# Optimization experiments

Hardware: AMD Instinct MI355X
Metric: run time of the kernel (lower is better)

The kernel has to match this reference:

```python
import jax, jax.numpy as jnp
import numpy as np
import math

N = 4096
E = 131072
D_IN = 148      # d_node_feat
D_HID = 128     # d_node_reshape (DIHGNN.d_node_feat)
D_OUT = 148     # d_output


def setup_inputs() -> dict:
    key = jax.random.key(0)
    ks = jax.random.split(key, 10)
    node_feat = jax.random.normal(ks[0], (1, N, D_IN), dtype=jnp.float32)
    edge_index = jax.random.randint(ks[1], (2, E), 0, N, dtype=jnp.int64)
    # learned parameters
    W1 = jax.random.normal(ks[2], (D_HID, D_IN), dtype=jnp.float32) * 0.02
    b1 = jnp.zeros((D_HID,), dtype=jnp.float32)
    a_param = jnp.array([0.9], dtype=jnp.float32)   # DIHGNN.a
    Wd = jax.random.normal(ks[3], (D_OUT, D_HID), dtype=jnp.float32) * 0.02
    bd = jnp.zeros((D_OUT,), dtype=jnp.float32)
    W2 = jax.random.normal(ks[4], (2, D_OUT), dtype=jnp.float32) * 0.02
    b2 = jnp.zeros((2,), dtype=jnp.float32)
    return {"node_feat": node_feat, "edge_index": edge_index, "num_node": N,
            "W1": W1, "b1": b1, "a_param": a_param, "Wd": Wd, "bd": bd,
            "W2": W2, "b2": b2}


def reference(node_feat, edge_index, num_node, W1, b1, a_param, Wd, bd, W2, b2):
    n = num_node
    x = node_feat[0]                                   # [N, D_IN]
    x = x @ W1.T + b1                                  # linear_1 -> [N, D_HID]

    # dense adjacency via scatter-set (duplicates collapse to 1, as in torch)
    adj = jnp.zeros((n, n), dtype=jnp.float32).at[edge_index[0], edge_index[1]].set(1.0)

    # asymmetric degree normalization: D_col^{-1/2} A D_row^{-1/2}
    L = adj.sum(axis=0)                                # column sums
    R = adj.sum(axis=1)                                # row sums
    L_is = jnp.where(L > 0, jax.lax.rsqrt(jnp.maximum(L, 1e-30)), 0.0)
    R_is = jnp.where(R > 0, jax.lax.rsqrt(jnp.maximum(R, 1e-30)), 0.0)
    adj_norm = L_is[:, None] * adj * R_is[None, :]

    # custom tanh: 0.5 + 0.5 * tanh(2 * a)
    alpha = 0.5 + 0.5 * jnp.tanh(2.0 * a_param[0])     # scalar

    # graph diffusion: (I - alpha * A_norm)^{-1} x, as a linear solve
    eye = jnp.eye(n, dtype=jnp.float32)
    x = jnp.linalg.solve(eye - alpha * adj_norm, x)    # [N, D_HID]

    x = x @ Wd.T + bd                                  # DIHGNN.linear -> [N, D_OUT]

    # similarity loss (scaled by DIHGNN.d_node_feat = D_HID)
    sim = (x @ x.T) / math.sqrt(D_HID)                 # [N, N]
    sim = sim * (1.0 - eye)                            # zero diagonal
    sim = jax.nn.relu(sim)
    loss = sim.sum() / (n * (n - 1))

    x = x * (1.0 - alpha)
    x = jax.nn.relu(x)
    pooled = jnp.max(x, axis=0, keepdims=True)         # global_max_pool, single graph -> [1, D_OUT]
    out = pooled @ W2.T + b2                           # [1, 2]
    return (out, loss)
```

## Files before the change

### kernel.cpp

```cpp
#include <hip/hip_runtime.h>
#include <hip/hip_bf16.h>
#include <math.h>

#define N_NODES 4096
#define N_EDGES 131072
#define BCAP 80
#define DIN 148
#define DHID 128
#define DOUT 148
#define KP 160
#define NITER 6

typedef __attribute__((ext_vector_type(8))) _Float16 half8;
typedef __attribute__((ext_vector_type(4))) float f32x4;

__device__ inline float h2f(unsigned e) {
    union { unsigned short u; _Float16 h; } cv;
    cv.u = (unsigned short)(e & 0xffffu);
    return (float)cv.h;
}
__device__ inline float2 h2f2(unsigned p) {
    union { unsigned u; _Float16 h[2]; } cv; cv.u = p;
    return make_float2((float)cv.h[0], (float)cv.h[1]);
}
__device__ inline unsigned f2h2(float x, float y) {
    union { unsigned u; _Float16 h[2]; } cv;
    cv.h[0] = (_Float16)x; cv.h[1] = (_Float16)y;
    return cv.u;
}

__global__ __launch_bounds__(256) void prep_kernel(const int* __restrict__ ei,
                                                   const float* __restrict__ W1,
                                                   const float* __restrict__ Wd,
                                                   float* __restrict__ W1T,
                                                   float* __restrict__ WdT,
                                                   unsigned* __restrict__ bitmap,
                                                   unsigned* __restrict__ bucket,
                                                   int* __restrict__ rowdeg,
                                                   int* __restrict__ coldeg) {
    int gtid = blockIdx.x * 256 + threadIdx.x;
    if (gtid < DIN * DHID) {
        int kk = gtid >> 7, d = gtid & 127;
        W1T[gtid] = W1[d * DIN + kk];
    } else if (gtid < DIN * DHID + DHID * DOUT) {
        int i2 = gtid - DIN * DHID;
        int h = i2 / DOUT, o = i2 - h * DOUT;
        WdT[i2] = Wd[o * DHID + h];
    }
    int i = ei[gtid] & (N_NODES - 1);
    int j = ei[gtid + N_EDGES] & (N_NODES - 1);
    unsigned pos = (unsigned)i * (unsigned)N_NODES + (unsigned)j;
    unsigned w = pos >> 5, m = 1u << (pos & 31u);
    unsigned old = atomicOr(&bitmap[w], m);
    if (!(old & m)) {
        int p = atomicAdd(&rowdeg[i], 1);
        if (p < BCAP) bucket[i * BCAP + p] = (unsigned)j;
        atomicAdd(&coldeg[j], 1);
    }
}

__global__ __launch_bounds__(256) void finalize_kernel(unsigned* __restrict__ bucket,
                                                       const int* __restrict__ rowdeg,
                                                       const int* __restrict__ coldeg,
                                                       float* __restrict__ acoef,
                                                       const float* __restrict__ a_param,
                                                       const float* __restrict__ nf,
                                                       const float* __restrict__ W1T,
                                                       const float* __restrict__ b1,
                                                       float* __restrict__ Bm,
                                                       unsigned* __restrict__ Bh) {
    int tid = threadIdx.x, bid = blockIdx.x;
    int r0 = bid * 16;
    for (int idx = tid; idx < 16 * BCAP; idx += 256) {
        int r = r0 + idx / BCAP, q = idx % BCAP;
        int dg = min(rowdeg[r], BCAP);
        if (q < dg) {
            unsigned col = bucket[r * BCAP + q];
            int rd = rowdeg[col];
            float rsj = (rd > 0) ? rsqrtf((float)rd) : 0.0f;
            union { _Float16 h; unsigned short u; } cv;
            cv.h = (_Float16)rsj;
            bucket[r * BCAP + q] = (col << 16) | (unsigned)cv.u;
        }
    }
    if (tid < 16) {
        int r = r0 + tid;
        float alpha = 0.5f + 0.5f * tanhf(2.0f * a_param[0]);
        int cd = coldeg[r];
        acoef[r] = (cd > 0) ? alpha * rsqrtf((float)cd) : 0.0f;
    }
    __shared__ float sA[16 * 152];
    __shared__ float sB[16 * 128];
    for (int idx = tid; idx < 16 * DIN; idx += 256) {
        int nd = idx / DIN, c = idx - nd * DIN;
        sA[nd * 152 + c] = nf[(r0 + nd) * DIN + c];
    }
    __syncthreads();
    int half = tid >> 7, d = tid & 127;
    float a[8];
#pragma unroll
    for (int n = 0; n < 8; ++n) a[n] = 0.f;
    const float* sb8 = sA + half * 8 * 152;
    for (int kk = 0; kk < DIN; ++kk) {
        float wv = W1T[kk * DHID + d];
#pragma unroll
        for (int n = 0; n < 8; ++n) a[n] += sb8[n * 152 + kk] * wv;
    }
    float bb = b1[d];
#pragma unroll
    for (int n = 0; n < 8; ++n) {
        int nd = half * 8 + n;
        float v = a[n] + bb;
        Bm[(r0 + nd) * DHID + d] = v;
        sB[nd * 128 + d] = v;
    }
    __syncthreads();
    for (int idx = tid; idx < 16 * 64; idx += 256) {
        int nd = idx >> 6, dp = idx & 63;
        Bh[(r0 + nd) * 64 + dp] = f2h2(sB[nd * 128 + 2 * dp], sB[nd * 128 + 2 * dp + 1]);
    }
}

template<bool INH, bool OUTH, bool LAST>
__global__ __launch_bounds__(256) void spmv_kernel(const void* __restrict__ xin_,
                                                   void* __restrict__ xout_,
                                                   const float* __restrict__ Bm,
                                                   const float* __restrict__ prev2,
                                                   const unsigned* __restrict__ cc,
                                                   const int* __restrict__ rowdeg,
                                                   const float* __restrict__ acoef,
                                                   double* __restrict__ accd) {
    int tid = threadIdx.x;
    int wid = __builtin_amdgcn_readfirstlane(tid >> 6);
    int lane = tid & 63;
    int r = blockIdx.x * 4 + wid;
    int dg8 = (min(rowdeg[r], BCAP) + 7) & ~7;
    int nch = dg8 >> 3;
    const uint4* __restrict__ q = (const uint4*)(cc + r * BCAP);
    const unsigned* __restrict__ xh = (const unsigned*)xin_;
    const float2* __restrict__ x2 = (const float2*)xin_;
    auto ldx = [&](unsigned e) -> float2 {
        int col = (int)(e >> 16);
        if constexpr (INH) return h2f2(xh[col * 64 + lane]);
        else return x2[col * 64 + lane];
    };
    float ax = 0.f, ay = 0.f;
    uint4 qa0 = q[0], qb0 = q[1];
    float2 v0 = ldx(qa0.x), v1 = ldx(qa0.y), v2 = ldx(qa0.z), v3 = ldx(qa0.w);
    float2 v4 = ldx(qb0.x), v5 = ldx(qb0.y), v6 = ldx(qb0.z), v7 = ldx(qb0.w);
    uint4 qa1 = q[2], qb1 = q[3];
    for (int c = 0; c < nch; ++c) {
        float2 w0 = ldx(qa1.x), w1 = ldx(qa1.y), w2 = ldx(qa1.z), w3 = ldx(qa1.w);
        float2 w4 = ldx(qb1.x), w5 = ldx(qb1.y), w6 = ldx(qb1.z), w7 = ldx(qb1.w);
        uint4 na = q[2 * c + 4], nb = q[2 * c + 5];
        float c0 = h2f(qa0.x), c1 = h2f(qa0.y), c2f = h2f(qa0.z), c3 = h2f(qa0.w);
        float c4 = h2f(qb0.x), c5 = h2f(qb0.y), c6 = h2f(qb0.z), c7 = h2f(qb0.w);
        ax += c0 * v0.x + c1 * v1.x + c2f * v2.x + c3 * v3.x
            + c4 * v4.x + c5 * v5.x + c6 * v6.x + c7 * v7.x;
        ay += c0 * v0.y + c1 * v1.y + c2f * v2.y + c3 * v3.y
            + c4 * v4.y + c5 * v5.y + c6 * v6.y + c7 * v7.y;
        qa0 = qa1; qb0 = qb1; qa1 = na; qb1 = nb;
        v0 = w0; v1 = w1; v2 = w2; v3 = w3;
        v4 = w4; v5 = w5; v6 = w6; v7 = w7;
    }
    float ac = acoef[r];
    int idx = r * 64 + lane;
    float2 b = ((const float2*)Bm)[idx];
    float vx = b.x + ac * ax, vy = b.y + ac * ay;
    if constexpr (OUTH) {
        ((unsigned*)xout_)[idx] = f2h2(vx, vy);
    } else {
        ((float2*)xout_)[idx] = make_float2(vx, vy);
    }
    if constexpr (LAST) {
        float2 xp = ((const float2*)xin_)[idx];
        float2 p2 = ((const float2*)prev2)[idx];
        float dpx = xp.x - p2.x, dpy = xp.y - p2.y;
        float dnx = vx - xp.x, dny = vy - xp.y;
        double s0 = (double)dpx * dpx + (double)dpy * dpy;
        double s1 = (double)dnx * dpx + (double)dny * dpy;
        __shared__ double sh0[256], sh1[256];
        sh0[tid] = s0; sh1[tid] = s1;
        __syncthreads();
        for (int off = 128; off > 0; off >>= 1) {
            if (tid < off) { sh0[tid] += sh0[tid + off]; sh1[tid] += sh1[tid + off]; }
            __syncthreads();
        }
        if (tid == 0) { atomicAdd(&accd[1], sh0[0]); atomicAdd(&accd[2], sh1[0]); }
    }
}

__global__ __launch_bounds__(256) void post_kernel(const float* __restrict__ last,
                                                   const float* __restrict__ prev,
                                                   const double* __restrict__ accd,
                                                   const float* __restrict__ WdT,
                                                   const float* __restrict__ bd,
                                                   _Float16* __restrict__ yH,
                                                   unsigned* __restrict__ mcolu) {
    int tid = threadIdx.x, bid = blockIdx.x;
    int r0 = bid * 16;
    double d0 = accd[1], d1 = accd[2];
    float lam = (d0 > 0.0) ? (float)(d1 / d0) : 0.0f;
    float den = 1.0f - lam;
    if (fabsf(den) < 1e-4f) den = (den < 0.0f) ? -1e-4f : 1e-4f;
    float sf = fminf(fmaxf(lam / den, -1e4f), 1e4f);
    __shared__ float sx[16 * DHID];
    for (int idx = tid; idx < 16 * DHID; idx += 256) {
        int node = r0 + (idx >> 7), ccol = idx & 127;
        float l = last[node * DHID + ccol];
        sx[idx] = l + sf * (l - prev[node * DHID + ccol]);
    }
    __syncthreads();
    for (int idx = tid; idx < 16 * (KP - DOUT); idx += 256) {
        int node = r0 + idx / (KP - DOUT);
        int ccol = DOUT + idx % (KP - DOUT);
        yH[node * KP + ccol] = (_Float16)0.0f;
    }
    if (tid < DOUT) {
        float acc[16];
#pragma unroll
        for (int nd = 0; nd < 16; ++nd) acc[nd] = 0.f;
        for (int h = 0; h < DHID; ++h) {
            float wv = WdT[h * DOUT + tid];
#pragma unroll
            for (int nd = 0; nd < 16; ++nd) acc[nd] += sx[nd * DHID + h] * wv;
        }
        float bb = bd[tid];
        float lm = 0.0f;
#pragma unroll
        for (int nd = 0; nd < 16; ++nd) {
            float v = acc[nd] + bb;
            yH[(r0 + nd) * KP + tid] = (_Float16)v;
            lm = fmaxf(lm, v);
        }
        atomicMax(&mcolu[tid], __float_as_uint(lm));
    }
}

__global__ __launch_bounds__(256) void simloss_kernel(const _Float16* __restrict__ yH,
                                                      double* __restrict__ accd,
                                                      unsigned* __restrict__ cnt,
                                                      const unsigned* __restrict__ mcolu,
                                                      const float* __restrict__ W2,
                                                      const float* __restrict__ b2,
                                                      const float* __restrict__ a_param,
                                                      float* __restrict__ out) {
    int tid = threadIdx.x;
    int tb = blockIdx.x;
    int ti = 0, rem = tb;
    while (rem >= 32 - ti) { rem -= 32 - ti; ++ti; }
    int tj = ti + rem;
    int wid = tid >> 6, lane = tid & 63;
    int wr = wid >> 1, wc = wid & 1;
    int fr = lane & 15, kq = lane >> 4;
    const half8* __restrict__ ap =
        (const half8*)(yH + (size_t)(ti * 128 + wr * 64 + fr) * KP);
    const half8* __restrict__ bp =
        (const half8*)(yH + (size_t)(tj * 128 + wc * 64 + fr) * KP);
    f32x4 C[4][4];
#pragma unroll
    for (int m = 0; m < 4; ++m)
#pragma unroll
        for (int n = 0; n < 4; ++n) C[m][n] = (f32x4)0.0f;
#pragma unroll
    for (int kk = 0; kk < KP / 32; ++kk) {
        half8 a[4], bf[4];
#pragma unroll
        for (int m = 0; m < 4; ++m) a[m] = ap[m * 320 + kk * 4 + kq];
#pragma unroll
        for (int n = 0; n < 4; ++n) bf[n] = bp[n * 320 + kk * 4 + kq];
#pragma unroll
        for (int m = 0; m < 4; ++m)
#pragma unroll
            for (int n = 0; n < 4; ++n)
                C[m][n] = __builtin_amdgcn_mfma_f32_16x16x32_f16(a[m], bf[n], C[m][n], 0, 0, 0);
    }
    const float inv = 0.0883883476483184405f;
    float wgt = (ti == tj) ? 1.0f : 2.0f;
    float lsum = 0.0f;
    int rq = kq * 4;
#pragma unroll
    for (int m = 0; m < 4; ++m)
#pragma unroll
        for (int n = 0; n < 4; ++n)
#pragma unroll
            for (int reg = 0; reg < 4; ++reg) {
                int gi = ti * 128 + wr * 64 + m * 16 + rq + reg;
                int gj = tj * 128 + wc * 64 + n * 16 + fr;
                float v = C[m][n][reg] * inv;
                if (gi != gj && v > 0.0f) lsum += wgt * v;
            }
    for (int o2 = 32; o2 > 0; o2 >>= 1) lsum += __shfl_down(lsum, o2);
    __shared__ float ws[4];
    __shared__ bool lastblk;
    if ((tid & 63) == 0) ws[tid >> 6] = lsum;
    __syncthreads();
    if (tid == 0) {
        atomicAdd(&accd[0], (double)(ws[0] + ws[1] + ws[2] + ws[3]));
        __threadfence();
        unsigned r = __hip_atomic_fetch_add(&cnt[1], 1u, __ATOMIC_ACQ_REL,
                                            __HIP_MEMORY_SCOPE_AGENT);
        lastblk = (r == 527u);
    }
    __syncthreads();
    if (lastblk && tid < 64) {
        float alpha = 0.5f + 0.5f * tanhf(2.0f * a_param[0]);
        float oma = 1.0f - alpha;
        float s0 = 0.0f, s1 = 0.0f;
        for (int o = tid; o < DOUT; o += 64) {
            float p = __uint_as_float(mcolu[o]);
            s0 += p * W2[o];
            s1 += p * W2[DOUT + o];
        }
        for (int off = 32; off > 0; off >>= 1) {
            s0 += __shfl_down(s0, off);
            s1 += __shfl_down(s1, off);
        }
        if (tid == 0) {
            double loss = __hip_atomic_load(&accd[0], __ATOMIC_RELAXED,
                                            __HIP_MEMORY_SCOPE_AGENT);
            out[0] = b2[0] + oma * s0;
            out[1] = b2[1] + oma * s1;
            out[2] = (float)(loss / (4096.0 * 4095.0));
        }
    }
}

extern "C" void kernel_launch(void* const* d_in, const int* in_sizes, int n_in,
                              void* d_out, int out_size, void* d_ws, size_t ws_size,
                              hipStream_t stream) {
    (void)in_sizes; (void)n_in; (void)out_size; (void)ws_size;
    const float* node_feat  = (const float*)d_in[0];
    const int*   edge_index = (const int*)d_in[1];
    const float* W1         = (const float*)d_in[3];
    const float* b1         = (const float*)d_in[4];
    const float* a_param    = (const float*)d_in[5];
    const float* Wd         = (const float*)d_in[6];
    const float* bd         = (const float*)d_in[7];
    const float* W2         = (const float*)d_in[8];
    const float* b2         = (const float*)d_in[9];
    float*       out        = (float*)d_out;

    char* w = (char*)d_ws;
    size_t off = 0;
    auto alloc = [&](size_t bytes) -> char* {
        char* p = w + off;
        off = (off + bytes + 255) & ~(size_t)255;
        return p;
    };
    double*   accd    = (double*)   alloc(8 * sizeof(double));
    unsigned* cnt     = (unsigned*) alloc(16 * sizeof(unsigned));
    int*      rowdeg  = (int*)      alloc(N_NODES * 4);
    int*      coldeg  = (int*)      alloc(N_NODES * 4);
    unsigned* mcolu   = (unsigned*) alloc(256 * 4);
    unsigned* bitmap  = (unsigned*) alloc((size_t)N_NODES * N_NODES / 8);
    unsigned* bucket  = (unsigned*) alloc((size_t)N_NODES * BCAP * 4 + 1024);
    size_t zero_end = off;
    float*    acoef   = (float*)    alloc(N_NODES * 4);
    float*    W1T     = (float*)    alloc(DIN * DHID * 4);
    float*    WdT     = (float*)    alloc(DHID * DOUT * 4);
    float*    Bm      = (float*)    alloc(N_NODES * DHID * 4);
    unsigned* Bh      = (unsigned*) alloc((size_t)N_NODES * 64 * 4);
    unsigned* H0      = (unsigned*) alloc((size_t)N_NODES * 64 * 4);
    unsigned* H1      = (unsigned*) alloc((size_t)N_NODES * 64 * 4);
    float*    Y0      = (float*)    alloc(N_NODES * DHID * 4);
    float*    Y1      = (float*)    alloc(N_NODES * DHID * 4);
    float*    Y2      = (float*)    alloc(N_NODES * DHID * 4);
    _Float16* yH      = (_Float16*) alloc((size_t)N_NODES * KP * 2);

    hipMemsetAsync(w, 0, zero_end, stream);

    prep_kernel<<<N_EDGES / 256, 256, 0, stream>>>(edge_index, W1, Wd, W1T, WdT,
                                                   bitmap, bucket, rowdeg, coldeg);
    finalize_kernel<<<N_NODES / 16, 256, 0, stream>>>(bucket, rowdeg, coldeg, acoef,
                                                      a_param, node_feat, W1T, b1, Bm, Bh);

    const int GB = N_NODES / 4;
    spmv_kernel<true,  true,  false><<<GB, 256, 0, stream>>>(Bh, H0, Bm, nullptr, bucket, rowdeg, acoef, accd);
    spmv_kernel<true,  true,  false><<<GB, 256, 0, stream>>>(H0, H1, Bm, nullptr, bucket, rowdeg, acoef, accd);
    spmv_kernel<true,  true,  false><<<GB, 256, 0, stream>>>(H1, H0, Bm, nullptr, bucket, rowdeg, acoef, accd);
    spmv_kernel<true,  false, false><<<GB, 256, 0, stream>>>(H0, Y0, Bm, nullptr, bucket, rowdeg, acoef, accd);
    spmv_kernel<false, false, false><<<GB, 256, 0, stream>>>(Y0, Y1, Bm, nullptr, bucket, rowdeg, acoef, accd);
    spmv_kernel<false, false, true ><<<GB, 256, 0, stream>>>(Y1, Y2, Bm, Y0, bucket, rowdeg, acoef, accd);

    post_kernel<<<N_NODES / 16, 256, 0, stream>>>(Y2, Y1, accd, WdT, bd, yH, mcolu);
    simloss_kernel<<<528, 256, 0, stream>>>(yH, accd, cnt, mcolu, W2, b2, a_param, out);
}
```

Measured before the change: 157.3 us.

## Fuse finalize into prep kernel and compute normalization coefficients inside SpMV

```diff
diff --git a/kernel.cpp b/kernel.cpp
--- a/kernel.cpp
+++ b/kernel.cpp
@@ -9,16 +9,10 @@
 #define DHID 128
 #define DOUT 148
 #define KP 160
-#define NITER 6
 
 typedef __attribute__((ext_vector_type(8))) _Float16 half8;
 typedef __attribute__((ext_vector_type(4))) float f32x4;
 
-__device__ inline float h2f(unsigned e) {
-    union { unsigned short u; _Float16 h; } cv;
-    cv.u = (unsigned short)(e & 0xffffu);
-    return (float)cv.h;
-}
 __device__ inline float2 h2f2(unsigned p) {
     union { unsigned u; _Float16 h[2]; } cv; cv.u = p;
     return make_float2((float)cv.h[0], (float)cv.h[1]);
@@ -28,152 +22,142 @@
     cv.h[0] = (_Float16)x; cv.h[1] = (_Float16)y;
     return cv.u;
 }
+__device__ inline float2 cvtx(unsigned g) { return h2f2(g); }
+__device__ inline float2 cvtx(float2 g)   { return g; }
 
 __global__ __launch_bounds__(256) void prep_kernel(const int* __restrict__ ei,
                                                    const float* __restrict__ W1,
                                                    const float* __restrict__ Wd,
-                                                   float* __restrict__ W1T,
+                                                   const float* __restrict__ b1,
+                                                   const float* __restrict__ nf,
                                                    float* __restrict__ WdT,
                                                    unsigned* __restrict__ bitmap,
                                                    unsigned* __restrict__ bucket,
                                                    int* __restrict__ rowdeg,
-                                                   int* __restrict__ coldeg) {
-    int gtid = blockIdx.x * 256 + threadIdx.x;
-    if (gtid < DIN * DHID) {
-        int kk = gtid >> 7, d = gtid & 127;
-        W1T[gtid] = W1[d * DIN + kk];
-    } else if (gtid < DIN * DHID + DHID * DOUT) {
-        int i2 = gtid - DIN * DHID;
-        int h = i2 / DOUT, o = i2 - h * DOUT;
-        WdT[i2] = Wd[o * DHID + h];
-    }
-    int i = ei[gtid] & (N_NODES - 1);
-    int j = ei[gtid + N_EDGES] & (N_NODES - 1);
-    unsigned pos = (unsigned)i * (unsigned)N_NODES + (unsigned)j;
-    unsigned w = pos >> 5, m = 1u << (pos & 31u);
-    unsigned old = atomicOr(&bitmap[w], m);
-    if (!(old & m)) {
-        int p = atomicAdd(&rowdeg[i], 1);
-        if (p < BCAP) bucket[i * BCAP + p] = (unsigned)j;
-        atomicAdd(&coldeg[j], 1);
-    }
-}
-
-__global__ __launch_bounds__(256) void finalize_kernel(unsigned* __restrict__ bucket,
-                                                       const int* __restrict__ rowdeg,
-                                                       const int* __restrict__ coldeg,
-                                                       float* __restrict__ acoef,
-                                                       const float* __restrict__ a_param,
-                                                       const float* __restrict__ nf,
-                                                       const float* __restrict__ W1T,
-                                                       const float* __restrict__ b1,
-                                                       float* __restrict__ Bm,
-                                                       unsigned* __restrict__ Bh) {
+                                                   int* __restrict__ coldeg,
+                                                   float* __restrict__ Bm,
+                                                   unsigned* __restrict__ Bh) {
     int tid = threadIdx.x, bid = blockIdx.x;
-    int r0 = bid * 16;
-    for (int idx = tid; idx < 16 * BCAP; idx += 256) {
-        int r = r0 + idx / BCAP, q = idx % BCAP;
-        int dg = min(rowdeg[r], BCAP);
-        if (q < dg) {
-            unsigned col = bucket[r * BCAP + q];
-            int rd = rowdeg[col];
-            float rsj = (rd > 0) ? rsqrtf((float)rd) : 0.0f;
-            union { _Float16 h; unsigned short u; } cv;
-            cv.h = (_Float16)rsj;
-            bucket[r * BCAP + q] = (col << 16) | (unsigned)cv.u;
-        }
-    }
-    if (tid < 16) {
-        int r = r0 + tid;
-        float alpha = 0.5f + 0.5f * tanhf(2.0f * a_param[0]);
-        int cd = coldeg[r];
-        acoef[r] = (cd > 0) ? alpha * rsqrtf((float)cd) : 0.0f;
+    int gtid = bid * 256 + tid;
+    if (gtid < DHID * DOUT) {
+        int h = gtid / DOUT, o = gtid - h * DOUT;
+        WdT[gtid] = Wd[o * DHID + h];
+    }
+    {
+        int i = ei[gtid] & (N_NODES - 1);
+        int j = ei[gtid + N_EDGES] & (N_NODES - 1);
+        unsigned pos = (unsigned)i * (unsigned)N_NODES + (unsigned)j;
+        unsigned w = pos >> 5, m = 1u << (pos & 31u);
+        unsigned old = atomicOr(&bitmap[w], m);
+        if (!(old & m)) {
+            int p = atomicAdd(&rowdeg[i], 1);
+            if (p < BCAP) bucket[i * BCAP + p] = (unsigned)j;
+            atomicAdd(&coldeg[j], 1);
+        }
     }
     __shared__ float sA[16 * 152];
     __shared__ float sB[16 * 128];
-    for (int idx = tid; idx < 16 * DIN; idx += 256) {
-        int nd = idx / DIN, c = idx - nd * DIN;
-        sA[nd * 152 + c] = nf[(r0 + nd) * DIN + c];
-    }
-    __syncthreads();
-    int half = tid >> 7, d = tid & 127;
-    float a[8];
-#pragma unroll
-    for (int n = 0; n < 8; ++n) a[n] = 0.f;
-    const float* sb8 = sA + half * 8 * 152;
-    for (int kk = 0; kk < DIN; ++kk) {
-        float wv = W1T[kk * DHID + d];
-#pragma unroll
-        for (int n = 0; n < 8; ++n) a[n] += sb8[n * 152 + kk] * wv;
-    }
-    float bb = b1[d];
-#pragma unroll
-    for (int n = 0; n < 8; ++n) {
-        int nd = half * 8 + n;
-        float v = a[n] + bb;
-        Bm[(r0 + nd) * DHID + d] = v;
-        sB[nd * 128 + d] = v;
-    }
-    __syncthreads();
-    for (int idx = tid; idx < 16 * 64; idx += 256) {
-        int nd = idx >> 6, dp = idx & 63;
-        Bh[(r0 + nd) * 64 + dp] = f2h2(sB[nd * 128 + 2 * dp], sB[nd * 128 + 2 * dp + 1]);
-    }
-}
-
-template<bool INH, bool OUTH, bool LAST>
+    if ((bid & 1) == 0) {
+        int r0 = (bid >> 1) * 16;
+        for (int idx = tid; idx < 16 * DIN; idx += 256) {
+            int nd = idx / DIN, c = idx - nd * DIN;
+            sA[nd * 152 + c] = nf[(r0 + nd) * DIN + c];
+        }
+        __syncthreads();
+        int half = tid >> 7, d = tid & 127;
+        float a[8];
+#pragma unroll
+        for (int n = 0; n < 8; ++n) a[n] = 0.f;
+        const float* __restrict__ wrow = W1 + d * DIN;
+        const float* sb8 = sA + half * 8 * 152;
+        for (int kk = 0; kk < DIN; ++kk) {
+            float wv = wrow[kk];
+#pragma unroll
+            for (int n = 0; n < 8; ++n) a[n] += sb8[n * 152 + kk] * wv;
+        }
+        float bb = b1[d];
+#pragma unroll
+        for (int n = 0; n < 8; ++n) {
+            int nd = half * 8 + n;
+            float v = a[n] + bb;
+            Bm[(r0 + nd) * DHID + d] = v;
+            sB[nd * 128 + d] = v;
+        }
+        __syncthreads();
+        for (int idx = tid; idx < 16 * 64; idx += 256) {
+            int nd = idx >> 6, dp = idx & 63;
+            Bh[(r0 + nd) * 64 + dp] = f2h2(sB[nd * 128 + 2 * dp], sB[nd * 128 + 2 * dp + 1]);
+        }
+    }
+}
+
+template<bool INH, bool DUAL, bool LAST>
 __global__ __launch_bounds__(256) void spmv_kernel(const void* __restrict__ xin_,
-                                                   void* __restrict__ xout_,
+                                                   unsigned* __restrict__ xoutH,
+                                                   float* __restrict__ xoutF,
                                                    const float* __restrict__ Bm,
                                                    const float* __restrict__ prev2,
                                                    const unsigned* __restrict__ cc,
                                                    const int* __restrict__ rowdeg,
-                                                   const float* __restrict__ acoef,
+                                                   const int* __restrict__ coldeg,
+                                                   const float* __restrict__ a_param,
                                                    double* __restrict__ accd) {
     int tid = threadIdx.x;
     int wid = __builtin_amdgcn_readfirstlane(tid >> 6);
     int lane = tid & 63;
     int r = blockIdx.x * 4 + wid;
-    int dg8 = (min(rowdeg[r], BCAP) + 7) & ~7;
-    int nch = dg8 >> 3;
+    int dg = min(rowdeg[r], BCAP);
+    int nch = (dg + 7) >> 3;
+    float alpha = 0.5f + 0.5f * tanhf(2.0f * a_param[0]);
+    int cdg = coldeg[r];
+    float ac = (cdg > 0) ? alpha * rsqrtf((float)cdg) : 0.0f;
     const uint4* __restrict__ q = (const uint4*)(cc + r * BCAP);
     const unsigned* __restrict__ xh = (const unsigned*)xin_;
-    const float2* __restrict__ x2 = (const float2*)xin_;
-    auto ldx = [&](unsigned e) -> float2 {
-        int col = (int)(e >> 16);
-        if constexpr (INH) return h2f2(xh[col * 64 + lane]);
-        else return x2[col * 64 + lane];
+    const float2* __restrict__ x2f = (const float2*)xin_;
+    auto ld = [&](unsigned col) {
+        if constexpr (INH) return xh[col * 64 + lane];
+        else               return x2f[col * 64 + lane];
     };
     float ax = 0.f, ay = 0.f;
-    uint4 qa0 = q[0], qb0 = q[1];
-    float2 v0 = ldx(qa0.x), v1 = ldx(qa0.y), v2 = ldx(qa0.z), v3 = ldx(qa0.w);
-    float2 v4 = ldx(qb0.x), v5 = ldx(qb0.y), v6 = ldx(qb0.z), v7 = ldx(qb0.w);
-    uint4 qa1 = q[2], qb1 = q[3];
+    uint4 ca = q[0], cb = q[1];
+    auto g0 = ld(ca.x), g1 = ld(ca.y), g2 = ld(ca.z), g3 = ld(ca.w);
+    auto g4 = ld(cb.x), g5 = ld(cb.y), g6 = ld(cb.z), g7 = ld(cb.w);
+    int d0 = rowdeg[ca.x], d1 = rowdeg[ca.y], d2 = rowdeg[ca.z], d3 = rowdeg[ca.w];
+    int d4 = rowdeg[cb.x], d5 = rowdeg[cb.y], d6 = rowdeg[cb.z], d7 = rowdeg[cb.w];
+    uint4 na = q[2], nb = q[3];
     for (int c = 0; c < nch; ++c) {
-        float2 w0 = ldx(qa1.x), w1 = ldx(qa1.y), w2 = ldx(qa1.z), w3 = ldx(qa1.w);
-        float2 w4 = ldx(qb1.x), w5 = ldx(qb1.y), w6 = ldx(qb1.z), w7 = ldx(qb1.w);
-        uint4 na = q[2 * c + 4], nb = q[2 * c + 5];
-        float c0 = h2f(qa0.x), c1 = h2f(qa0.y), c2f = h2f(qa0.z), c3 = h2f(qa0.w);
-        float c4 = h2f(qb0.x), c5 = h2f(qb0.y), c6 = h2f(qb0.z), c7 = h2f(qb0.w);
-        ax += c0 * v0.x + c1 * v1.x + c2f * v2.x + c3 * v3.x
-            + c4 * v4.x + c5 * v5.x + c6 * v6.x + c7 * v7.x;
-        ay += c0 * v0.y + c1 * v1.y + c2f * v2.y + c3 * v3.y
-            + c4 * v4.y + c5 * v5.y + c6 * v6.y + c7 * v7.y;
-        qa0 = qa1; qb0 = qb1; qa1 = na; qb1 = nb;
-        v0 = w0; v1 = w1; v2 = w2; v3 = w3;
-        v4 = w4; v5 = w5; v6 = w6; v7 = w7;
-    }
-    float ac = acoef[r];
+        auto h0 = ld(na.x), h1 = ld(na.y), h2 = ld(na.z), h3 = ld(na.w);
+        auto h4 = ld(nb.x), h5 = ld(nb.y), h6 = ld(nb.z), h7 = ld(nb.w);
+        int e0 = rowdeg[na.x], e1 = rowdeg[na.y], e2 = rowdeg[na.z], e3 = rowdeg[na.w];
+        int e4 = rowdeg[nb.x], e5 = rowdeg[nb.y], e6 = rowdeg[nb.z], e7 = rowdeg[nb.w];
+        uint4 fa = q[2 * c + 4], fb = q[2 * c + 5];
+        int t = c * 8;
+        float2 x0 = cvtx(g0), x1 = cvtx(g1), x2 = cvtx(g2), x3 = cvtx(g3);
+        float2 x4 = cvtx(g4), x5 = cvtx(g5), x6 = cvtx(g6), x7 = cvtx(g7);
+        float c0 = (t + 0 < dg && d0 > 0) ? rsqrtf((float)d0) : 0.f;
+        float c1 = (t + 1 < dg && d1 > 0) ? rsqrtf((float)d1) : 0.f;
+        float c2 = (t + 2 < dg && d2 > 0) ? rsqrtf((float)d2) : 0.f;
+        float c3 = (t + 3 < dg && d3 > 0) ? rsqrtf((float)d3) : 0.f;
+        float c4 = (t + 4 < dg && d4 > 0) ? rsqrtf((float)d4) : 0.f;
+        float c5 = (t + 5 < dg && d5 > 0) ? rsqrtf((float)d5) : 0.f;
+        float c6 = (t + 6 < dg && d6 > 0) ? rsqrtf((float)d6) : 0.f;
+        float c7 = (t + 7 < dg && d7 > 0) ? rsqrtf((float)d7) : 0.f;
+        ax += c0 * x0.x + c1 * x1.x + c2 * x2.x + c3 * x3.x
+            + c4 * x4.x + c5 * x5.x + c6 * x6.x + c7 * x7.x;
+        ay += c0 * x0.y + c1 * x1.y + c2 * x2.y + c3 * x3.y
+            + c4 * x4.y + c5 * x5.y + c6 * x6.y + c7 * x7.y;
+        g0 = h0; g1 = h1; g2 = h2; g3 = h3;
+        g4 = h4; g5 = h5; g6 = h6; g7 = h7;
+        d0 = e0; d1 = e1; d2 = e2; d3 = e3;
+        d4 = e4; d5 = e5; d6 = e6; d7 = e7;
+        na = fa; nb = fb;
+    }
     int idx = r * 64 + lane;
     float2 b = ((const float2*)Bm)[idx];
     float vx = b.x + ac * ax, vy = b.y + ac * ay;
-    if constexpr (OUTH) {
-        ((unsigned*)xout_)[idx] = f2h2(vx, vy);
-    } else {
-        ((float2*)xout_)[idx] = make_float2(vx, vy);
-    }
     if constexpr (LAST) {
-        float2 xp = ((const float2*)xin_)[idx];
+        ((float2*)xoutF)[idx] = make_float2(vx, vy);
+        float2 xp = x2f[idx];
         float2 p2 = ((const float2*)prev2)[idx];
         float dpx = xp.x - p2.x, dpy = xp.y - p2.y;
         float dnx = vx - xp.x, dny = vy - xp.y;
@@ -187,6 +171,9 @@
             __syncthreads();
         }
         if (tid == 0) { atomicAdd(&accd[1], sh0[0]); atomicAdd(&accd[2], sh1[0]); }
+    } else {
+        xoutH[idx] = f2h2(vx, vy);
+        if constexpr (DUAL) ((float2*)xoutF)[idx] = make_float2(vx, vy);
     }
 }
 
@@ -356,8 +343,6 @@
     unsigned* bitmap  = (unsigned*) alloc((size_t)N_NODES * N_NODES / 8);
     unsigned* bucket  = (unsigned*) alloc((size_t)N_NODES * BCAP * 4 + 1024);
     size_t zero_end = off;
-    float*    acoef   = (float*)    alloc(N_NODES * 4);
-    float*    W1T     = (float*)    alloc(DIN * DHID * 4);
     float*    WdT     = (float*)    alloc(DHID * DOUT * 4);
     float*    Bm      = (float*)    alloc(N_NODES * DHID * 4);
     unsigned* Bh      = (unsigned*) alloc((size_t)N_NODES * 64 * 4);
@@ -370,18 +355,17 @@
 
     hipMemsetAsync(w, 0, zero_end, stream);
 
-    prep_kernel<<<N_EDGES / 256, 256, 0, stream>>>(edge_index, W1, Wd, W1T, WdT,
-                                                   bitmap, bucket, rowdeg, coldeg);
-    finalize_kernel<<<N_NODES / 16, 256, 0, stream>>>(bucket, rowdeg, coldeg, acoef,
-                                                      a_param, node_feat, W1T, b1, Bm, Bh);
+    prep_kernel<<<N_EDGES / 256, 256, 0, stream>>>(edge_index, W1, Wd, b1, node_feat,
+                                                   WdT, bitmap, bucket, rowdeg, coldeg,
+                                                   Bm, Bh);
 
     const int GB = N_NODES / 4;
-    spmv_kernel<true,  true,  false><<<GB, 256, 0, stream>>>(Bh, H0, Bm, nullptr, bucket, rowdeg, acoef, accd);
-    spmv_kernel<true,  true,  false><<<GB, 256, 0, stream>>>(H0, H1, Bm, nullptr, bucket, rowdeg, acoef, accd);
-    spmv_kernel<true,  true,  false><<<GB, 256, 0, stream>>>(H1, H0, Bm, nullptr, bucket, rowdeg, acoef, accd);
-    spmv_kernel<true,  false, false><<<GB, 256, 0, stream>>>(H0, Y0, Bm, nullptr, bucket, rowdeg, acoef, accd);
-    spmv_kernel<false, false, false><<<GB, 256, 0, stream>>>(Y0, Y1, Bm, nullptr, bucket, rowdeg, acoef, accd);
-    spmv_kernel<false, false, true ><<<GB, 256, 0, stream>>>(Y1, Y2, Bm, Y0, bucket, rowdeg, acoef, accd);
+    spmv_kernel<true,  false, false><<<GB, 256, 0, stream>>>(Bh, H0, nullptr, Bm, nullptr, bucket, rowdeg, coldeg, a_param, accd);
+    spmv_kernel<true,  false, false><<<GB, 256, 0, stream>>>(H0, H1, nullptr, Bm, nullptr, bucket, rowdeg, coldeg, a_param, accd);
+    spmv_kernel<true,  false, false><<<GB, 256, 0, stream>>>(H1, H0, nullptr, Bm, nullptr, bucket, rowdeg, coldeg, a_param, accd);
+    spmv_kernel<true,  true,  false><<<GB, 256, 0, stream>>>(H0, H1, Y0, Bm, nullptr, bucket, rowdeg, coldeg, a_param, accd);
+    spmv_kernel<true,  true,  false><<<GB, 256, 0, stream>>>(H1, H0, Y1, Bm, nullptr, bucket, rowdeg, coldeg, a_param, accd);
+    spmv_kernel<false, false, true ><<<GB, 256, 0, stream>>>(Y1, nullptr, Y2, Bm, Y0, bucket, rowdeg, coldeg, a_param, accd);
 
     post_kernel<<<N_NODES / 16, 256, 0, stream>>>(Y2, Y1, accd, WdT, bd, yH, mcolu);
     simloss_kernel<<<528, 256, 0, stream>>>(yH, accd, cnt, mcolu, W2, b2, a_param, out);
```

New measurement: 166.4 us. 5.8% more time.
